# Optimization experiments

Hardware: AMD Instinct MI355X
Metric: run time of the kernel (lower is better)

The kernel has to match this reference:

```python
import jax, jax.numpy as jnp
from jax import lax
import numpy as np

B, C, L = 32, 8, 512
C_IN = 512      # must equal L (tokenConv consumes permuted tensor)
D_MODEL = 512
SCALE_NUM = 64  # 63 actual scales


def build_wavelet_bank(scale_num, LB=-8.0, UB=8.0, N=1024, Fb=2.0, Fc=8.0):
    """Replicates cmor_torch; returns centered zero-padded kernel bank [S, K].
    Zero-centering is exact because every kernel length (16*s+1) is odd and K is odd,
    so the padded conv with pad=(K-1)//2 equals the original per-scale conv with
    pad=(k-1)//2."""
    x = np.linspace(LB, UB, N)
    wav = (np.pi * Fb) ** (-0.5) * np.exp(2j * np.pi * Fc * x) * np.exp(-x ** 2 / Fb)
    step = x[1] - x[0]
    kernels = []
    for scale in np.arange(1, scale_num):
        j = (np.arange(scale * (x[-1] - x[0]) + 1) / (scale * step)).astype(int)
        j = j[j < wav.size]
        kernels.append(np.real(wav[j]) * scale ** (-0.5))
    K = max(len(k) for k in kernels)
    if K % 2 == 0:
        K += 1
    bank = np.zeros((len(kernels), K), np.float32)
    for i, k in enumerate(kernels):
        assert (K - len(k)) % 2 == 0, "kernel parity mismatch"
        off = (K - len(k)) // 2
        bank[i, off:off + len(k)] = k
    return bank


def setup_inputs() -> dict:
    key = jax.random.key(0)
    k1, k2 = jax.random.split(key)
    x = jax.random.normal(k1, (B, C, L), dtype=jnp.float32)
    wavelet_bank = jnp.asarray(build_wavelet_bank(SCALE_NUM))  # [63, K]
    token_w = jax.random.normal(k2, (D_MODEL, C_IN, 3), dtype=jnp.float32) * 0.02
    return {"x": x, "wavelet_bank": wavelet_bank, "token_w": token_w}


def reference(x, wavelet_bank, token_w):
    Bb, Cc, Ll = x.shape
    S, K = wavelet_bank.shape
    pad = (K - 1) // 2
    # fused CWT over all (channel, scale) pairs: [B*C, 1, L] conv [S, 1, K] -> [B*C, S, L]
    xr = x.reshape(Bb * Cc, 1, Ll)
    conv = lax.conv_general_dilated(
        xr, wavelet_bank[:, None, :], window_strides=(1,),
        padding=[(pad, pad)], dimension_numbers=("NCH", "OIH", "NCH"))
    d = jnp.abs(jnp.diff(conv, axis=-1))                 # [B*C, S, L-1]
    d = jnp.concatenate([d, d[..., -1:]], axis=-1)       # replicate last sample -> L
    feats = d.reshape(Bb, Cc * S, Ll)
    out = jnp.concatenate([x, feats], axis=1)            # [B, C*(1+S), L]
    # tokenConv on permuted tensor: channels = L (= c_in), length = C*(1+S)
    h = out.transpose(0, 2, 1)                           # [B, L, C_total]
    hp = jnp.concatenate([h[..., -1:], h, h[..., :1]], axis=-1)  # circular pad=1
    y = lax.conv_general_dilated(
        hp, token_w, window_strides=(1,), padding="VALID",
        dimension_numbers=("NCH", "OIH", "NCH"))         # [B, d_model, C_total]
    return y.transpose(0, 2, 1)                          # [B, C_total, d_model]
```

## Files before the change

kernel.cpp:

```cpp
#include <hip/hip_runtime.h>
#include <hip/hip_bf16.h>

#define NB 32
#define NC 8
#define NL 512
#define NS 63
#define NK 1009
#define NPAD 504
#define ND 512
#define NCT 512
#define NROWS 514

typedef __attribute__((ext_vector_type(4))) float f32x4;
typedef __attribute__((ext_vector_type(8))) short short8;

#define APAD_BYTES (NB * NROWS * NL * 2)
#define WB_BYTES   (3 * ND * NL * 2)

typedef const __attribute__((address_space(1))) unsigned int* gp1_t;
typedef __attribute__((address_space(3))) unsigned int* lp3_t;
__device__ __forceinline__ void gload_lds16(const void* g, void* l) {
  __builtin_amdgcn_global_load_lds((gp1_t)g, (lp3_t)l, 16, 0, 0);
}

__device__ __forceinline__ unsigned short bf16_bits(float v) {
  return __builtin_bit_cast(unsigned short, __float2bfloat16(v));
}

#define WAITVM(N) asm volatile("s_waitcnt vmcnt(" #N ")" ::: "memory")
#define FENCE() asm volatile("" ::: "memory")
#define BAR() __builtin_amdgcn_s_barrier()
#define PRIO1() __builtin_amdgcn_s_setprio(1)
#define PRIO0() __builtin_amdgcn_s_setprio(0)

__global__ __launch_bounds__(256) void prep_kernel(
    const float* __restrict__ bank, const float* __restrict__ tw,
    __hip_bfloat16* __restrict__ Wb, __hip_bfloat16* __restrict__ bankB) {
  const int idx = blockIdx.x * 256 + threadIdx.x;

  {
    int i0 = idx * 4;
    const float4* t4 = (const float4*)(tw + (size_t)i0 * 3);
    float4 a = t4[0], bq = t4[1], c4 = t4[2];
    ushort4 w0 = make_ushort4(bf16_bits(a.x), bf16_bits(a.w), bf16_bits(bq.z), bf16_bits(c4.y));
    ushort4 w1 = make_ushort4(bf16_bits(a.y), bf16_bits(bq.x), bf16_bits(bq.w), bf16_bits(c4.z));
    ushort4 w2 = make_ushort4(bf16_bits(a.z), bf16_bits(bq.y), bf16_bits(c4.x), bf16_bits(c4.w));
    *(ushort4*)(Wb + 0 * ND * NL + i0) = w0;
    *(ushort4*)(Wb + 1 * ND * NL + i0) = w1;
    *(ushort4*)(Wb + 2 * ND * NL + i0) = w2;
  }
  {
    int s = idx >> 10, k = idx & 1023;
    float v = (s < NS && k < NK) ? bank[s * NK + k] : 0.f;
    bankB[idx] = __float2bfloat16(v);
  }
}

#define CPY8_STRIDE 3152

__global__ __launch_bounds__(512) void cwt_kernel(
    const float* __restrict__ x, const __hip_bfloat16* __restrict__ bankB,
    __hip_bfloat16* __restrict__ Apad) {
  __shared__ __align__(16) char smem[8 * 16384 + 8 * CPY8_STRIDE];
  char* bankS = smem;
  char* cpy = smem + 8 * 16384;

  const int tid = threadIdx.x;
  const int bc = blockIdx.x;
  const int b = bc >> 3, c = bc & 7;
  const int w = tid >> 6, l = tid & 63;
  const int hi = l >> 4, li = l & 15;
  const int r8 = l & 7;

  const float* xrow = x + bc * NL;

  if (tid < 512) {
    __hip_bfloat16 v = __float2bfloat16(xrow[tid]);
    Apad[((size_t)(b * NROWS) + 1 + c) * NL + tid] = v;
    if (c == 0) Apad[((size_t)(b * NROWS) + 513) * NL + tid] = v;
  }

  for (int i = 0; i < 13; ++i) {
    int p = tid + i * 512;
    if (p < 6176) {
      int r_ = p / 772;
      int pe = p - r_ * 772;
      int g0 = 2 * pe;
      int i0 = g0 - 8 + r_;
      float xa = (i0 >= NPAD && i0 < NPAD + NL) ? xrow[i0 - NPAD] : 0.f;
      float xb = (i0 + 1 >= NPAD && i0 + 1 < NPAD + NL) ? xrow[i0 + 1 - NPAD] : 0.f;
      float xc = (i0 + 2 >= NPAD && i0 + 2 < NPAD + NL) ? xrow[i0 + 2 - NPAD] : 0.f;
      unsigned u = (unsigned)bf16_bits(xb - xa) | ((unsigned)bf16_bits(xc - xb) << 16);
      *(unsigned*)(cpy + r_ * CPY8_STRIDE + g0 * 2) = u;
    }
  }

#define STAGE(kt)                                                             \
  {                                                                           \
    for (int i = 0; i < 2; ++i) {                                             \
      int ck = tid + i * 512;                                                 \
      int s_ = ck >> 4, rb = ck & 15;                                         \
      int srcc = rb ^ (s_ & 7);                                               \
      gload_lds16(bankB + s_ * 1024 + (kt) * 128 + srcc * 8,                  \
                  bankS + (kt) * 16384 + ck * 16);                            \
    }                                                                         \
  }

#define AVMM(kt, ksl, m)                                                       \
  {                                                                            \
    int srow = (m) * 16 + li;                                                  \
    int chunk = ((ksl) * 4 + hi) ^ (srow & 7);                                 \
    short8 av = *(const short8*)(bankS + (kt) * 16384 + srow * 256 + chunk * 16); \
    _Pragma("unroll") for (int n = 0; n < 4; ++n)                              \
      acc[m][n] = __builtin_amdgcn_mfma_f32_16x16x32_bf16(av, bv[n],           \
                                                          acc[m][n], 0, 0, 0); \
  }

#define CCOMP(kt, M0, M1, M2, M3)                                              \
  {                                                                            \
    _Pragma("unroll") for (int ksl = 0; ksl < 4; ++ksl) {                      \
      short8 bv[4];                                                            \
      _Pragma("unroll") for (int n = 0; n < 4; ++n) {                          \
        int ebyte = 16 + 2 * (tbase + n * 16 + 8 * (li >> 3) +                 \
                              (kt) * 128 + ksl * 32 + 8 * hi);                 \
        bv[n] = *(const short8*)(cpy + r8 * CPY8_STRIDE + ebyte);              \
      }                                                                        \
      if (M0) AVMM(kt, ksl, 0);                                                \
      if (M1) AVMM(kt, ksl, 1);                                                \
      if (M2) AVMM(kt, ksl, 2);                                                \
      if (M3) AVMM(kt, ksl, 3);                                                \
    }                                                                          \
  }

  STAGE(0); STAGE(1); STAGE(2); STAGE(3);
  STAGE(4); STAGE(5); STAGE(6); STAGE(7);

  f32x4 acc[4][4] = {};
  const int tbase = w * 64;

  asm volatile("s_waitcnt vmcnt(14) lgkmcnt(0)" ::: "memory");
  BAR(); FENCE(); CCOMP(0, 0, 0, 1, 1);
  WAITVM(12); BAR(); FENCE(); CCOMP(1, 0, 1, 1, 1);
  WAITVM(10); BAR(); FENCE(); CCOMP(2, 1, 1, 1, 1);
  WAITVM(8);  BAR(); FENCE(); CCOMP(3, 1, 1, 1, 1);
  WAITVM(6);  BAR(); FENCE(); CCOMP(4, 1, 1, 1, 1);
  WAITVM(4);  BAR(); FENCE(); CCOMP(5, 0, 1, 1, 1);
  WAITVM(2);  BAR(); FENCE(); CCOMP(6, 0, 0, 1, 1);
  WAITVM(0);  BAR(); FENCE(); CCOMP(7, 0, 0, 0, 1);

#pragma unroll
  for (int m = 0; m < 4; ++m) {
#pragma unroll
    for (int rg = 0; rg < 4; ++rg) {
      int s = m * 16 + hi * 4 + rg;
      if (s >= NS) continue;
      int ch = 8 + c * NS + s;
      size_t rowbase = ((size_t)(b * NROWS) + 1 + ch) * NL;
#pragma unroll
      for (int n = 0; n < 4; ++n) {
        int t = tbase + n * 16 + li;
        float d = fabsf(acc[m][n][rg]);
        __hip_bfloat16 hv = __float2bfloat16(d);
        bool lastgrp = (w == 7 && n == 3);
        bool skip = lastgrp && (li == 15);
        bool dup = lastgrp && (li == 14);
        if (!skip) Apad[rowbase + t] = hv;
        if (dup) Apad[rowbase + 511] = hv;
        if (ch == NCT - 1) {
          size_t wrapbase = (size_t)(b * NROWS) * NL;
          if (!skip) Apad[wrapbase + t] = hv;
          if (dup) Apad[wrapbase + 511] = hv;
        }
      }
    }
  }
#undef STAGE
#undef AVMM
#undef CCOMP
}

__global__ __launch_bounds__(512) void gemm_kernel(
    const __hip_bfloat16* __restrict__ Ap, const __hip_bfloat16* __restrict__ Wb,
    float* __restrict__ out) {
  __shared__ __hip_bfloat16 sA[3][256 * 64];
  __shared__ __hip_bfloat16 sB[3][128 * 64];

  const int tid = threadIdx.x;
  const int gid = blockIdx.x;
  const int idx = gid >> 3;
  const int mblk = (gid & 7) * 8 + (idx & 7);
  const int nblk = idx >> 3;
  const int b = mblk >> 1;
  const int p0 = (mblk & 1) * 256;
  const int o0 = nblk * 128;

  const int w = tid >> 6, lane = tid & 63;
  const int wm = w >> 1, wn = w & 1;
  const int row_in = lane & 15, hi = lane >> 4;

#define GSTAGE_H0(kt, bu)                                                      \
  {                                                                            \
    const int kap_ = (kt) >> 3;                                                \
    const int l0_ = ((kt) & 7) << 6;                                           \
    _Pragma("unroll") for (int i = 0; i < 2; ++i) {                            \
      int ck = tid + i * 512;                                                  \
      int row = ck >> 3, cg = (ck & 7) ^ (row & 7);                            \
      gload_lds16(Ap + ((b * NROWS + p0 + kap_ + row) * NL + l0_ + cg * 8),    \
                  &sA[bu][ck * 8]);                                            \
    }                                                                          \
    {                                                                          \
      int ck = tid;                                                            \
      int row = ck >> 3, cg = (ck & 7) ^ (row & 7);                            \
      gload_lds16(Wb + ((kap_ * ND + o0 + row) * NL + l0_ + cg * 8),           \
                  &sB[bu][ck * 8]);                                            \
    }                                                                          \
  }

#define GSTAGE_H1(kt, bu)                                                      \
  {                                                                            \
    const int kap_ = (kt) >> 3;                                                \
    const int l0_ = ((kt) & 7) << 6;                                           \
    _Pragma("unroll") for (int i = 2; i < 4; ++i) {                            \
      int ck = tid + i * 512;                                                  \
      int row = ck >> 3, cg = (ck & 7) ^ (row & 7);                            \
      gload_lds16(Ap + ((b * NROWS + p0 + kap_ + row) * NL + l0_ + cg * 8),    \
                  &sA[bu][ck * 8]);                                            \
    }                                                                          \
    {                                                                          \
      int ck = tid + 512;                                                      \
      int row = ck >> 3, cg = (ck & 7) ^ (row & 7);                            \
      gload_lds16(Wb + ((kap_ * ND + o0 + row) * NL + l0_ + cg * 8),           \
                  &sB[bu][ck * 8]);                                            \
    }                                                                          \
  }

#define SLICE(bu, ks, STG)                                                     \
  {                                                                            \
    short8 av[4], bv[4];                                                       \
    _Pragma("unroll") for (int m = 0; m < 4; ++m) {                            \
      int row = wm * 64 + m * 16 + row_in;                                     \
      int cs = ((ks) * 4 + hi) ^ (row & 7);                                    \
      av[m] = *(const short8*)(&sA[bu][(row * 8 + cs) * 8]);                   \
    }                                                                          \
    _Pragma("unroll") for (int n = 0; n < 4; ++n) {                            \
      int row = wn * 64 + n * 16 + row_in;                                     \
      int cs = ((ks) * 4 + hi) ^ (row & 7);                                    \
      bv[n] = *(const short8*)(&sB[bu][(row * 8 + cs) * 8]);                   \
    }                                                                          \
    STG;                                                                       \
    PRIO1();                                                                   \
    _Pragma("unroll") for (int m = 0; m < 4; ++m)                              \
      _Pragma("unroll") for (int n = 0; n < 4; ++n)                            \
        acc[m][n] = __builtin_amdgcn_mfma_f32_16x16x32_bf16(av[m], bv[n],      \
                                                            acc[m][n], 0, 0, 0); \
    PRIO0();                                                                   \
  }

#define STEP(kt, bu, bs)                                                       \
  WAITVM(6); BAR(); FENCE();                                                   \
  SLICE(bu, 0, GSTAGE_H0((kt) + 2, bs));                                       \
  SLICE(bu, 1, GSTAGE_H1((kt) + 2, bs));                                       \
  FENCE();

  f32x4 acc[4][4] = {};

  GSTAGE_H0(0, 0); GSTAGE_H1(0, 0);
  GSTAGE_H0(1, 1); GSTAGE_H1(1, 1);

  for (int g = 0; g < 7; ++g) {
    const int kt = g * 3;
    STEP(kt + 0, 0, 2);
    STEP(kt + 1, 1, 0);
    STEP(kt + 2, 2, 1);
  }
  STEP(21, 0, 2);
  WAITVM(6); BAR(); FENCE(); SLICE(1, 0, (void)0); SLICE(1, 1, (void)0); FENCE();
  WAITVM(0); BAR(); FENCE(); SLICE(2, 0, (void)0); SLICE(2, 1, (void)0);
#undef GSTAGE_H0
#undef GSTAGE_H1
#undef SLICE
#undef STEP

#pragma unroll
  for (int m = 0; m < 4; ++m) {
    const int p = p0 + wm * 64 + m * 16 + hi * 4;
#pragma unroll
    for (int n = 0; n < 4; ++n) {
      const int o = o0 + wn * 64 + n * 16 + row_in;
#pragma unroll
      for (int r = 0; r < 4; ++r)
        out[(size_t)((b * NCT) + p + r) * ND + o] = acc[m][n][r];
    }
  }
}

extern "C" void kernel_launch(void* const* d_in, const int* in_sizes, int n_in,
                              void* d_out, int out_size, void* d_ws, size_t ws_size,
                              hipStream_t stream) {
  const float* x = (const float*)d_in[0];
  const float* bank = (const float*)d_in[1];
  const float* tw = (const float*)d_in[2];
  float* out = (float*)d_out;

  char* ws = (char*)d_ws;
  __hip_bfloat16* Apad = (__hip_bfloat16*)ws;
  __hip_bfloat16* Wb = (__hip_bfloat16*)(ws + APAD_BYTES);
  __hip_bfloat16* bankB = (__hip_bfloat16*)(ws + APAD_BYTES + WB_BYTES);

  prep_kernel<<<256, 256, 0, stream>>>(bank, tw, Wb, bankB);
  cwt_kernel<<<256, 512, 0, stream>>>(x, bankB, Apad);
  gemm_kernel<<<256, 512, 0, stream>>>(Apad, Wb, out);
}
```

Measured before the change: 56.76 us.

## Use triple-buffered bank staging in CWT kernel and reuse sliding Toeplitz fragments

Cuts the CWT kernel's LDS bank buffer from eight stages to a rotating three-buffer ring, issuing each stage's async global-to-LDS load while computing on earlier stages. It adds a launch-bounds occupancy hint of four and restructures the B-operand loads so overlapping Toeplitz fragments are shared across k-slices, loading 10 vectors instead of 16 per k-tile. The aim is to raise occupancy through lower LDS use and to reduce LDS read traffic. In exchange there are more barriers with reuse hazards, and the register cap may cause spills.

```diff
diff --git a/kernel.cpp b/kernel.cpp
--- a/kernel.cpp
+++ b/kernel.cpp
@@ -58,12 +58,12 @@
 
 #define CPY8_STRIDE 3152
 
-__global__ __launch_bounds__(512) void cwt_kernel(
+__global__ __launch_bounds__(512, 4) void cwt_kernel(
     const float* __restrict__ x, const __hip_bfloat16* __restrict__ bankB,
     __hip_bfloat16* __restrict__ Apad) {
-  __shared__ __align__(16) char smem[8 * 16384 + 8 * CPY8_STRIDE];
+  __shared__ __align__(16) char smem[3 * 16384 + 8 * CPY8_STRIDE];
   char* bankS = smem;
-  char* cpy = smem + 8 * 16384;
+  char* cpy = smem + 3 * 16384;
 
   const int tid = threadIdx.x;
   const int bc = blockIdx.x;
@@ -95,58 +95,71 @@
     }
   }
 
-#define STAGE(kt)                                                             \
+  WAITVM(0);
+
+#define STAGE(kt, bu)                                                         \
   {                                                                           \
     for (int i = 0; i < 2; ++i) {                                             \
       int ck = tid + i * 512;                                                 \
       int s_ = ck >> 4, rb = ck & 15;                                         \
       int srcc = rb ^ (s_ & 7);                                               \
       gload_lds16(bankB + s_ * 1024 + (kt) * 128 + srcc * 8,                  \
-                  bankS + (kt) * 16384 + ck * 16);                            \
+                  bankS + (bu) * 16384 + ck * 16);                            \
     }                                                                         \
   }
 
-#define AVMM(kt, ksl, m)                                                       \
+#define LDU(kt, i)                                                            \
+  (*(const short8*)(cpy + r8 * CPY8_STRIDE + 16 +                             \
+                    2 * (tbase + (i) * 16 + 8 * (li >> 3) + (kt) * 128 + 8 * hi)))
+
+#define AVMM4(kt, bu, ksl, m, B0, B1, B2, B3)                                  \
   {                                                                            \
     int srow = (m) * 16 + li;                                                  \
     int chunk = ((ksl) * 4 + hi) ^ (srow & 7);                                 \
-    short8 av = *(const short8*)(bankS + (kt) * 16384 + srow * 256 + chunk * 16); \
-    _Pragma("unroll") for (int n = 0; n < 4; ++n)                              \
-      acc[m][n] = __builtin_amdgcn_mfma_f32_16x16x32_bf16(av, bv[n],           \
-                                                          acc[m][n], 0, 0, 0); \
-  }
-
-#define CCOMP(kt, M0, M1, M2, M3)                                              \
-  {                                                                            \
-    _Pragma("unroll") for (int ksl = 0; ksl < 4; ++ksl) {                      \
-      short8 bv[4];                                                            \
-      _Pragma("unroll") for (int n = 0; n < 4; ++n) {                          \
-        int ebyte = 16 + 2 * (tbase + n * 16 + 8 * (li >> 3) +                 \
-                              (kt) * 128 + ksl * 32 + 8 * hi);                 \
-        bv[n] = *(const short8*)(cpy + r8 * CPY8_STRIDE + ebyte);              \
-      }                                                                        \
-      if (M0) AVMM(kt, ksl, 0);                                                \
-      if (M1) AVMM(kt, ksl, 1);                                                \
-      if (M2) AVMM(kt, ksl, 2);                                                \
-      if (M3) AVMM(kt, ksl, 3);                                                \
-    }                                                                          \
-  }
-
-  STAGE(0); STAGE(1); STAGE(2); STAGE(3);
-  STAGE(4); STAGE(5); STAGE(6); STAGE(7);
+    short8 av = *(const short8*)(bankS + (bu) * 16384 + srow * 256 + chunk * 16); \
+    acc[m][0] = __builtin_amdgcn_mfma_f32_16x16x32_bf16(av, B0, acc[m][0], 0, 0, 0); \
+    acc[m][1] = __builtin_amdgcn_mfma_f32_16x16x32_bf16(av, B1, acc[m][1], 0, 0, 0); \
+    acc[m][2] = __builtin_amdgcn_mfma_f32_16x16x32_bf16(av, B2, acc[m][2], 0, 0, 0); \
+    acc[m][3] = __builtin_amdgcn_mfma_f32_16x16x32_bf16(av, B3, acc[m][3], 0, 0, 0); \
+  }
+
+#define CCOMP(kt, bu, M0, M1, M2, M3)                                          \
+  {                                                                            \
+    short8 q0 = LDU(kt, 0), q1 = LDU(kt, 1), q2 = LDU(kt, 2);                  \
+    short8 q3 = LDU(kt, 3), q4 = LDU(kt, 4), q5 = LDU(kt, 5);                  \
+    if (M0) AVMM4(kt, bu, 0, 0, q0, q1, q2, q3);                               \
+    if (M1) AVMM4(kt, bu, 0, 1, q0, q1, q2, q3);                               \
+    if (M2) AVMM4(kt, bu, 0, 2, q0, q1, q2, q3);                               \
+    if (M3) AVMM4(kt, bu, 0, 3, q0, q1, q2, q3);                               \
+    if (M0) AVMM4(kt, bu, 1, 0, q2, q3, q4, q5);                               \
+    if (M1) AVMM4(kt, bu, 1, 1, q2, q3, q4, q5);                               \
+    if (M2) AVMM4(kt, bu, 1, 2, q2, q3, q4, q5);                               \
+    if (M3) AVMM4(kt, bu, 1, 3, q2, q3, q4, q5);                               \
+    q0 = LDU(kt, 6); q1 = LDU(kt, 7); q2 = LDU(kt, 8); q3 = LDU(kt, 9);        \
+    if (M0) AVMM4(kt, bu, 2, 0, q4, q5, q0, q1);                               \
+    if (M1) AVMM4(kt, bu, 2, 1, q4, q5, q0, q1);                               \
+    if (M2) AVMM4(kt, bu, 2, 2, q4, q5, q0, q1);                               \
+    if (M3) AVMM4(kt, bu, 2, 3, q4, q5, q0, q1);                               \
+    if (M0) AVMM4(kt, bu, 3, 0, q0, q1, q2, q3);                               \
+    if (M1) AVMM4(kt, bu, 3, 1, q0, q1, q2, q3);                               \
+    if (M2) AVMM4(kt, bu, 3, 2, q0, q1, q2, q3);                               \
+    if (M3) AVMM4(kt, bu, 3, 3, q0, q1, q2, q3);                               \
+  }
 
   f32x4 acc[4][4] = {};
   const int tbase = w * 64;
 
-  asm volatile("s_waitcnt vmcnt(14) lgkmcnt(0)" ::: "memory");
-  BAR(); FENCE(); CCOMP(0, 0, 0, 1, 1);
-  WAITVM(12); BAR(); FENCE(); CCOMP(1, 0, 1, 1, 1);
-  WAITVM(10); BAR(); FENCE(); CCOMP(2, 1, 1, 1, 1);
-  WAITVM(8);  BAR(); FENCE(); CCOMP(3, 1, 1, 1, 1);
-  WAITVM(6);  BAR(); FENCE(); CCOMP(4, 1, 1, 1, 1);
-  WAITVM(4);  BAR(); FENCE(); CCOMP(5, 0, 1, 1, 1);
-  WAITVM(2);  BAR(); FENCE(); CCOMP(6, 0, 0, 1, 1);
-  WAITVM(0);  BAR(); FENCE(); CCOMP(7, 0, 0, 0, 1);
+  STAGE(0, 0); STAGE(1, 1);
+
+  asm volatile("s_waitcnt vmcnt(2) lgkmcnt(0)" ::: "memory");
+  BAR(); FENCE(); STAGE(2, 2); CCOMP(0, 0, 0, 0, 1, 1); FENCE();
+  WAITVM(2); BAR(); FENCE(); STAGE(3, 0); CCOMP(1, 1, 0, 1, 1, 1); FENCE();
+  WAITVM(2); BAR(); FENCE(); STAGE(4, 1); CCOMP(2, 2, 1, 1, 1, 1); FENCE();
+  WAITVM(2); BAR(); FENCE(); STAGE(5, 2); CCOMP(3, 0, 1, 1, 1, 1); FENCE();
+  WAITVM(2); BAR(); FENCE(); STAGE(6, 0); CCOMP(4, 1, 1, 1, 1, 1); FENCE();
+  WAITVM(2); BAR(); FENCE(); STAGE(7, 1); CCOMP(5, 2, 0, 1, 1, 1); FENCE();
+  WAITVM(2); BAR(); FENCE(); CCOMP(6, 0, 0, 0, 1, 1); FENCE();
+  WAITVM(0); BAR(); FENCE(); CCOMP(7, 1, 0, 0, 0, 1);
 
 #pragma unroll
   for (int m = 0; m < 4; ++m) {
@@ -175,7 +188,8 @@
     }
   }
 #undef STAGE
-#undef AVMM
+#undef LDU
+#undef AVMM4
 #undef CCOMP
 }
 
```

Result: no change. 56.23 us (-0.9%).
